# Optimization experiments

Measured on AMD Instinct MI355X. Metric: run time of the kernel, lower is better.

Reference implementation:

```python
import jax, jax.numpy as jnp
import numpy as np

LEAKY_SLOPE = 0.2

def leaky_relu(x):
    return jnp.where(x >= 0, x, LEAKY_SLOPE * x)

def setup_inputs() -> dict:
    key = jax.random.key(0)
    ks = jax.random.split(key, 11)
    B, F = 512, 1024
    H1, H2, OUT = 512, 256, 128  # hidden_dims = [512, 256, 128]
    KD = 5                        # minibatch kernel dims
    x = jax.random.normal(ks[0], (B, F), dtype=jnp.float32)
    # features: Linear(F,H1) -> LReLU -> Linear(H1,H2) -> LReLU
    W1 = jax.random.normal(ks[1], (F, H1), dtype=jnp.float32) / np.sqrt(F)
    b1 = jnp.zeros((H1,), dtype=jnp.float32)
    W2 = jax.random.normal(ks[2], (H1, H2), dtype=jnp.float32) / np.sqrt(H1)
    b2 = jnp.zeros((H2,), dtype=jnp.float32)
    # minibatch discrimination tensor T: (in=H2, out=OUT, kernel=KD), N(0,1) init
    T = jax.random.normal(ks[3], (H2, OUT, KD), dtype=jnp.float32)
    # final: Linear(H2+OUT, OUT) -> LReLU -> Linear(OUT, 1)
    W3 = jax.random.normal(ks[4], (H2 + OUT, OUT), dtype=jnp.float32) / np.sqrt(H2 + OUT)
    b3 = jnp.zeros((OUT,), dtype=jnp.float32)
    W4 = jax.random.normal(ks[5], (OUT, 1), dtype=jnp.float32) / np.sqrt(OUT)
    b4 = jnp.zeros((1,), dtype=jnp.float32)
    return {"x": x, "W1": W1, "b1": b1, "W2": W2, "b2": b2,
            "T": T, "W3": W3, "b3": b3, "W4": W4, "b4": b4}

def reference(x, W1, b1, W2, b2, T, W3, b3, W4, b4):
    # MLP feature stack (dropout = identity in eval mode)
    h = leaky_relu(x @ W1 + b1)          # (B, 512)
    h = leaky_relu(h @ W2 + b2)          # (B, 256)
    # Minibatch discrimination
    in_f, out_f, kd = T.shape
    M = (h @ T.reshape(in_f, out_f * kd)).reshape(-1, out_f, kd)  # (B, out, kd)
    # pairwise L1 over kernel dim: (B, B, out)
    norm = jnp.abs(M[:, None, :, :] - M[None, :, :, :]).sum(-1)
    o_b = jnp.exp(-norm).sum(0) - 1.0    # (B, out); -1 removes self term
    z = jnp.concatenate([h, o_b], axis=1)  # (B, 256+128)
    z = leaky_relu(z @ W3 + b3)
    return z @ W4 + b4                    # (B, 1)
```

## Files before the change

kernel.cpp:

```cpp
#include <hip/hip_runtime.h>
#include <math.h>

#define B_   512
#define F_   1024
#define H1_  512
#define H2_  256
#define OUT_ 128
#define KD_  5
#define NT_  640
#define ZK_  384

typedef short bf16x8 __attribute__((ext_vector_type(8)));
typedef float f32x16 __attribute__((ext_vector_type(16)));

__device__ __forceinline__ float lrelu(float v) { return v >= 0.f ? v : 0.2f * v; }

__device__ __forceinline__ unsigned f2bf(float f) {
    unsigned u = __float_as_uint(f);
    return (u + 0x7fffu + ((u >> 16) & 1u)) >> 16;
}
__device__ __forceinline__ unsigned pack2bf(float a, float b) {
    return f2bf(a) | (f2bf(b) << 16);
}

__device__ __forceinline__ bf16x8 frag_bf16row(const unsigned short* p, int idx, int ld, int k) {
    return *(const bf16x8*)(p + (size_t)idx * ld + k);
}
__device__ __forceinline__ bf16x8 frag_f32row(const float* p, int idx, int ld, int k) {
    const float4 a = *(const float4*)(p + (size_t)idx * ld + k);
    const float4 b = *(const float4*)(p + (size_t)idx * ld + k + 4);
    union { unsigned u[4]; bf16x8 v; } cv;
    cv.u[0] = pack2bf(a.x, a.y); cv.u[1] = pack2bf(a.z, a.w);
    cv.u[2] = pack2bf(b.x, b.y); cv.u[3] = pack2bf(b.z, b.w);
    return cv.v;
}
__device__ __forceinline__ bf16x8 frag_f32col(const float* p, int idx, int ld, int k) {
    union { unsigned u[4]; bf16x8 v; } cv;
    #pragma unroll
    for (int jj = 0; jj < 4; ++jj)
        cv.u[jj] = pack2bf(p[(size_t)(k + 2 * jj) * ld + idx],
                           p[(size_t)(k + 2 * jj + 1) * ld + idx]);
    return cv.v;
}
__device__ __forceinline__ bf16x8 frag_concat(const unsigned short* h2b,
                                              const float* obA, const float* obB,
                                              int idx, int k) {
    if (k < H2_) return frag_bf16row(h2b, idx, H2_, k);
    const float* pa = obA + (size_t)idx * OUT_ + (k - H2_);
    const float* pb = obB + (size_t)idx * OUT_ + (k - H2_);
    union { unsigned u[4]; bf16x8 v; } cv;
    #pragma unroll
    for (int jj = 0; jj < 4; ++jj)
        cv.u[jj] = pack2bf(pa[2 * jj] + pb[2 * jj], pa[2 * jj + 1] + pb[2 * jj + 1]);
    return cv.v;
}

#define M_BF16ROW 0
#define M_F32ROW  1
#define M_F32COL  2

template<int WAVES, int KSLICE, int AMODE, int BMODE,
         bool RELU, bool HAS_BIAS, bool BF16_OUT>
__global__ __launch_bounds__(WAVES * 64)
void gemm_k(const void* __restrict__ Ap, const void* __restrict__ Bp,
            const float* __restrict__ bias, void* __restrict__ Cout,
            int M, int N, int LDA, int LDB)
{
    __shared__ float Red[WAVES * 1024];
    const int tid  = threadIdx.x;
    const int wav  = tid >> 6;
    const int lane = tid & 63;
    const int half = lane >> 5;
    const int mn   = lane & 31;
    const int m0   = blockIdx.y * 32;
    const int n0   = blockIdx.x * 32;

    f32x16 acc;
    #pragma unroll
    for (int i = 0; i < 16; ++i) acc[i] = 0.f;

    #pragma unroll
    for (int s = 0; s < KSLICE / 16; ++s) {
        const int k = wav * KSLICE + 16 * s + 8 * half;
        bf16x8 af, bf;
        if (AMODE == M_BF16ROW)      af = frag_bf16row((const unsigned short*)Ap, m0 + mn, LDA, k);
        else if (AMODE == M_F32ROW)  af = frag_f32row((const float*)Ap, m0 + mn, LDA, k);
        else                         af = frag_f32col((const float*)Ap, m0 + mn, LDA, k);
        if (BMODE == M_BF16ROW)      bf = frag_bf16row((const unsigned short*)Bp, n0 + mn, LDB, k);
        else                         bf = frag_f32col((const float*)Bp, n0 + mn, LDB, k);
        acc = __builtin_amdgcn_mfma_f32_32x32x16_bf16(af, bf, acc, 0, 0, 0);
    }

    #pragma unroll
    for (int r = 0; r < 16; ++r) {
        const int row = (r & 3) + 8 * (r >> 2) + 4 * half;
        Red[wav * 1024 + row * 32 + mn] = acc[r];
    }
    __syncthreads();

    if (tid < 256) {
        const int e0 = tid * 4, row = e0 >> 5, col = e0 & 31;
        float v[4];
        #pragma unroll
        for (int q = 0; q < 4; ++q) {
            float u = 0.f;
            #pragma unroll
            for (int w = 0; w < WAVES; ++w) u += Red[w * 1024 + e0 + q];
            if (HAS_BIAS) u += bias[n0 + col + q];
            if (RELU) u = lrelu(u);
            v[q] = u;
        }
        if (BF16_OUT) {
            uint2 o;
            o.x = pack2bf(v[0], v[1]); o.y = pack2bf(v[2], v[3]);
            *(uint2*)((unsigned short*)Cout + (size_t)(m0 + row) * N + n0 + col) = o;
        } else {
            *(float4*)((float*)Cout + (size_t)(m0 + row) * N + n0 + col) =
                make_float4(v[0], v[1], v[2], v[3]);
        }
    }
}

__global__ __launch_bounds__(128)
void disc_kernel(const float* __restrict__ Mt, float* __restrict__ obH)
{
    const int o  = blockIdx.x >> 3;
    const int jq = (blockIdx.x >> 1) & 3;
    const int ih = blockIdx.x & 1;
    const int t  = threadIdx.x;
    const int j  = jq * 128 + t;
    const int i0 = ih * 256;
    __shared__ float L[256 * 8];
    const float* base = Mt + (size_t)o * 5 * 512;
    #pragma unroll
    for (int k = 0; k < KD_; ++k) {
        L[t * 8 + k]         = base[k * 512 + i0 + t];
        L[(t + 128) * 8 + k] = base[k * 512 + i0 + t + 128];
    }
    const float mj0 = base[0 * 512 + j], mj1 = base[1 * 512 + j],
                mj2 = base[2 * 512 + j], mj3 = base[3 * 512 + j],
                mj4 = base[4 * 512 + j];
    __syncthreads();

    float acc0 = 0.f, acc1 = 0.f;
    #pragma unroll 4
    for (int i = 0; i < 256; i += 2) {
        {
            const float4 a = *(const float4*)&L[i * 8];
            const float n = fabsf(a.x - mj0) + fabsf(a.y - mj1) + fabsf(a.z - mj2)
                          + fabsf(a.w - mj3) + fabsf(L[i * 8 + 4] - mj4);
            acc0 += __expf(-n);
        }
        {
            const float4 a = *(const float4*)&L[(i + 1) * 8];
            const float n = fabsf(a.x - mj0) + fabsf(a.y - mj1) + fabsf(a.z - mj2)
                          + fabsf(a.w - mj3) + fabsf(L[(i + 1) * 8 + 4] - mj4);
            acc1 += __expf(-n);
        }
    }
    const float self = ((j >> 8) == ih) ? 1.f : 0.f;
    obH[(size_t)ih * B_ * OUT_ + (size_t)j * OUT_ + o] = acc0 + acc1 - self;
}

__global__ __launch_bounds__(256)
void gemm3_dot(const unsigned short* __restrict__ h2b,
               const float* __restrict__ obA, const float* __restrict__ obB,
               const float* __restrict__ W3, const float* __restrict__ b3,
               const float* __restrict__ W4, const float* __restrict__ b4,
               float* __restrict__ out)
{
    __shared__ float Red[32 * 128];
    const int tid  = threadIdx.x;
    const int w    = tid >> 6;
    const int lane = tid & 63;
    const int half = lane >> 5;
    const int mn   = lane & 31;
    const int m0   = blockIdx.x * 32;
    const int n0   = w * 32;

    f32x16 acc;
    #pragma unroll
    for (int i = 0; i < 16; ++i) acc[i] = 0.f;

    #pragma unroll
    for (int s = 0; s < ZK_ / 16; ++s) {
        const int k = 16 * s + 8 * half;
        const bf16x8 af = frag_concat(h2b, obA, obB, m0 + mn, k);
        const bf16x8 bf = frag_f32col(W3, n0 + mn, OUT_, k);
        acc = __builtin_amdgcn_mfma_f32_32x32x16_bf16(af, bf, acc, 0, 0, 0);
    }

    #pragma unroll
    for (int r = 0; r < 16; ++r) {
        const int row = (r & 3) + 8 * (r >> 2) + 4 * half;
        const int col = n0 + mn;
        Red[row * 128 + col] = lrelu(acc[r] + b3[col]);
    }
    __syncthreads();

    if (tid < 128) {
        const int row = tid >> 2, q = tid & 3;
        float a = 0.f;
        #pragma unroll
        for (int cc0 = 0; cc0 < 32; ++cc0) {
            const int cc = (cc0 + tid) & 31;
            a += Red[row * 128 + q * 32 + cc] * W4[q * 32 + cc];
        }
        a += __shfl_down(a, 2, 4);
        a += __shfl_down(a, 1, 4);
        if (q == 0) out[m0 + row] = a + b4[0];
    }
}

extern "C" void kernel_launch(void* const* d_in, const int* in_sizes, int n_in,
                              void* d_out, int out_size, void* d_ws, size_t ws_size,
                              hipStream_t stream) {
    const float* x  = (const float*)d_in[0];
    const float* W1 = (const float*)d_in[1];
    const float* b1 = (const float*)d_in[2];
    const float* W2 = (const float*)d_in[3];
    const float* b2 = (const float*)d_in[4];
    const float* T  = (const float*)d_in[5];
    const float* W3 = (const float*)d_in[6];
    const float* b3 = (const float*)d_in[7];
    const float* W4 = (const float*)d_in[8];
    const float* b4 = (const float*)d_in[9];
    float* out = (float*)d_out;

    char* ws = (char*)d_ws;
    float*          Mt  = (float*)(ws + 0);
    float*          obH = (float*)(ws + 1310720);
    unsigned short* h1b = (unsigned short*)(ws + 1835008);
    unsigned short* h2b = (unsigned short*)(ws + 2359296);

    gemm_k<8, 128, M_F32ROW, M_F32COL, true, true, true>
        <<<dim3(H1_ / 32, B_ / 32), 512, 0, stream>>>(
        x, W1, b1, h1b, B_, H1_, F_, H1_);

    gemm_k<8, 64, M_BF16ROW, M_F32COL, true, true, true>
        <<<dim3(H2_ / 32, B_ / 32), 512, 0, stream>>>(
        h1b, W2, b2, h2b, B_, H2_, H1_, H2_);

    gemm_k<4, 64, M_F32COL, M_BF16ROW, false, false, false>
        <<<dim3(B_ / 32, NT_ / 32), 256, 0, stream>>>(
        T, h2b, nullptr, Mt, NT_, B_, NT_, H2_);

    disc_kernel<<<1024, 128, 0, stream>>>(Mt, obH);

    gemm3_dot<<<B_ / 32, 256, 0, stream>>>(
        h2b, obH, obH + B_ * OUT_, W3, b3, W4, b4, out);
}
```

Baseline: 109.3 us.

## Fuse all five stages into one cooperative persistent kernel with grid syncs

```diff
diff --git a/kernel.cpp b/kernel.cpp
--- a/kernel.cpp
+++ b/kernel.cpp
@@ -1,5 +1,8 @@
 #include <hip/hip_runtime.h>
+#include <hip/hip_cooperative_groups.h>
 #include <math.h>
+
+namespace cg = cooperative_groups;
 
 #define B_   512
 #define F_   1024
@@ -42,38 +45,22 @@
                            p[(size_t)(k + 2 * jj + 1) * ld + idx]);
     return cv.v;
 }
-__device__ __forceinline__ bf16x8 frag_concat(const unsigned short* h2b,
-                                              const float* obA, const float* obB,
-                                              int idx, int k) {
-    if (k < H2_) return frag_bf16row(h2b, idx, H2_, k);
-    const float* pa = obA + (size_t)idx * OUT_ + (k - H2_);
-    const float* pb = obB + (size_t)idx * OUT_ + (k - H2_);
-    union { unsigned u[4]; bf16x8 v; } cv;
-    #pragma unroll
-    for (int jj = 0; jj < 4; ++jj)
-        cv.u[jj] = pack2bf(pa[2 * jj] + pb[2 * jj], pa[2 * jj + 1] + pb[2 * jj + 1]);
-    return cv.v;
-}
 
 #define M_BF16ROW 0
 #define M_F32ROW  1
 #define M_F32COL  2
 
-template<int WAVES, int KSLICE, int AMODE, int BMODE,
-         bool RELU, bool HAS_BIAS, bool BF16_OUT>
-__global__ __launch_bounds__(WAVES * 64)
-void gemm_k(const void* __restrict__ Ap, const void* __restrict__ Bp,
-            const float* __restrict__ bias, void* __restrict__ Cout,
-            int M, int N, int LDA, int LDB)
-{
-    __shared__ float Red[WAVES * 1024];
-    const int tid  = threadIdx.x;
+template<int KSLICE, int AMODE, int BMODE, bool RELU, bool HAS_BIAS, bool BF16_OUT>
+__device__ __forceinline__
+void gemm_tile(float* Red,
+               const void* __restrict__ Ap, const void* __restrict__ Bp,
+               const float* __restrict__ bias, void* __restrict__ Cout,
+               int N, int LDA, int LDB, int m0, int n0, int tid)
+{
     const int wav  = tid >> 6;
     const int lane = tid & 63;
     const int half = lane >> 5;
     const int mn   = lane & 31;
-    const int m0   = blockIdx.y * 32;
-    const int n0   = blockIdx.x * 32;
 
     f32x16 acc;
     #pragma unroll
@@ -105,7 +92,7 @@
         for (int q = 0; q < 4; ++q) {
             float u = 0.f;
             #pragma unroll
-            for (int w = 0; w < WAVES; ++w) u += Red[w * 1024 + e0 + q];
+            for (int w = 0; w < 8; ++w) u += Red[w * 1024 + e0 + q];
             if (HAS_BIAS) u += bias[n0 + col + q];
             if (RELU) u = lrelu(u);
             v[q] = u;
@@ -119,73 +106,79 @@
                 make_float4(v[0], v[1], v[2], v[3]);
         }
     }
-}
-
-__global__ __launch_bounds__(128)
-void disc_kernel(const float* __restrict__ Mt, float* __restrict__ obH)
-{
-    const int o  = blockIdx.x >> 3;
-    const int jq = (blockIdx.x >> 1) & 3;
-    const int ih = blockIdx.x & 1;
-    const int t  = threadIdx.x;
-    const int j  = jq * 128 + t;
-    const int i0 = ih * 256;
-    __shared__ float L[256 * 8];
-    const float* base = Mt + (size_t)o * 5 * 512;
-    #pragma unroll
-    for (int k = 0; k < KD_; ++k) {
-        L[t * 8 + k]         = base[k * 512 + i0 + t];
-        L[(t + 128) * 8 + k] = base[k * 512 + i0 + t + 128];
-    }
+    __syncthreads();
+}
+
+__device__ __forceinline__
+void disc_phase(float* S, const float* __restrict__ Mt, float* __restrict__ obF,
+                int b, int tid)
+{
+    float* L = S;
+    float* P = S + 4096;
+    const int o  = b >> 1;
+    const int jh = b & 1;
+    const int t  = tid & 255;
+    const int ih = tid >> 8;
+    const float* base = Mt + (size_t)o * (KD_ * 512);
+
+    #pragma unroll
+    for (int k = 0; k < KD_; ++k)
+        L[tid * 8 + k] = base[k * 512 + tid];
+
+    const int j = jh * 256 + t;
     const float mj0 = base[0 * 512 + j], mj1 = base[1 * 512 + j],
                 mj2 = base[2 * 512 + j], mj3 = base[3 * 512 + j],
                 mj4 = base[4 * 512 + j];
     __syncthreads();
 
+    const int i0 = ih * 256;
     float acc0 = 0.f, acc1 = 0.f;
     #pragma unroll 4
     for (int i = 0; i < 256; i += 2) {
         {
-            const float4 a = *(const float4*)&L[i * 8];
+            const float4 a = *(const float4*)&L[(i0 + i) * 8];
             const float n = fabsf(a.x - mj0) + fabsf(a.y - mj1) + fabsf(a.z - mj2)
-                          + fabsf(a.w - mj3) + fabsf(L[i * 8 + 4] - mj4);
+                          + fabsf(a.w - mj3) + fabsf(L[(i0 + i) * 8 + 4] - mj4);
             acc0 += __expf(-n);
         }
         {
-            const float4 a = *(const float4*)&L[(i + 1) * 8];
+            const float4 a = *(const float4*)&L[(i0 + i + 1) * 8];
             const float n = fabsf(a.x - mj0) + fabsf(a.y - mj1) + fabsf(a.z - mj2)
-                          + fabsf(a.w - mj3) + fabsf(L[(i + 1) * 8 + 4] - mj4);
+                          + fabsf(a.w - mj3) + fabsf(L[(i0 + i + 1) * 8 + 4] - mj4);
             acc1 += __expf(-n);
         }
     }
-    const float self = ((j >> 8) == ih) ? 1.f : 0.f;
-    obH[(size_t)ih * B_ * OUT_ + (size_t)j * OUT_ + o] = acc0 + acc1 - self;
-}
-
-__global__ __launch_bounds__(256)
-void gemm3_dot(const unsigned short* __restrict__ h2b,
-               const float* __restrict__ obA, const float* __restrict__ obB,
-               const float* __restrict__ W3, const float* __restrict__ b3,
-               const float* __restrict__ W4, const float* __restrict__ b4,
-               float* __restrict__ out)
-{
-    __shared__ float Red[32 * 128];
-    const int tid  = threadIdx.x;
+    if (ih == 0) P[t] = acc0 + acc1;
+    __syncthreads();
+    if (ih == 1) obF[(size_t)o * B_ + j] = P[t] + acc0 + acc1 - 1.0f;
+    __syncthreads();
+}
+
+__device__ __forceinline__
+void final_phase(float* Red, const unsigned short* __restrict__ h2b,
+                 const float* __restrict__ obF,
+                 const float* __restrict__ W3, const float* __restrict__ b3,
+                 const float* __restrict__ W4, const float* __restrict__ b4,
+                 float* __restrict__ out, int m0, int tid)
+{
     const int w    = tid >> 6;
     const int lane = tid & 63;
     const int half = lane >> 5;
     const int mn   = lane & 31;
-    const int m0   = blockIdx.x * 32;
-    const int n0   = w * 32;
+    const int n0   = (w & 3) * 32;
+    const int kh   = w >> 2;
 
     f32x16 acc;
     #pragma unroll
     for (int i = 0; i < 16; ++i) acc[i] = 0.f;
 
     #pragma unroll
-    for (int s = 0; s < ZK_ / 16; ++s) {
-        const int k = 16 * s + 8 * half;
-        const bf16x8 af = frag_concat(h2b, obA, obB, m0 + mn, k);
+    for (int s = 0; s < 12; ++s) {
+        const int k = kh * 192 + 16 * s + 8 * half;
+        const int idx = m0 + mn;
+        bf16x8 af;
+        if (k < H2_) af = frag_bf16row(h2b, idx, H2_, k);
+        else         af = frag_f32col(obF, idx, B_, k - H2_);
         const bf16x8 bf = frag_f32col(W3, n0 + mn, OUT_, k);
         acc = __builtin_amdgcn_mfma_f32_32x32x16_bf16(af, bf, acc, 0, 0, 0);
     }
@@ -193,8 +186,7 @@
     #pragma unroll
     for (int r = 0; r < 16; ++r) {
         const int row = (r & 3) + 8 * (r >> 2) + 4 * half;
-        const int col = n0 + mn;
-        Red[row * 128 + col] = lrelu(acc[r] + b3[col]);
+        Red[kh * 4096 + row * 128 + n0 + mn] = acc[r];
     }
     __syncthreads();
 
@@ -204,12 +196,50 @@
         #pragma unroll
         for (int cc0 = 0; cc0 < 32; ++cc0) {
             const int cc = (cc0 + tid) & 31;
-            a += Red[row * 128 + q * 32 + cc] * W4[q * 32 + cc];
+            const int c = q * 32 + cc;
+            const float u = lrelu(Red[row * 128 + c] + Red[4096 + row * 128 + c] + b3[c]);
+            a += u * W4[c];
         }
         a += __shfl_down(a, 2, 4);
         a += __shfl_down(a, 1, 4);
         if (q == 0) out[m0 + row] = a + b4[0];
     }
+}
+
+__global__ __launch_bounds__(512)
+void mega(const float* __restrict__ x,  const float* __restrict__ W1, const float* __restrict__ b1,
+          const float* __restrict__ W2, const float* __restrict__ b2,
+          const float* __restrict__ T,
+          const float* __restrict__ W3, const float* __restrict__ b3,
+          const float* __restrict__ W4, const float* __restrict__ b4,
+          float* __restrict__ Mt, float* __restrict__ obF,
+          unsigned short* __restrict__ h1b, unsigned short* __restrict__ h2b,
+          float* __restrict__ out)
+{
+    __shared__ float S[8192];
+    cg::grid_group grid = cg::this_grid();
+    const int b   = blockIdx.x;
+    const int tid = threadIdx.x;
+
+    gemm_tile<128, M_F32ROW, M_F32COL, true, true, true>(
+        S, x, W1, b1, h1b, H1_, F_, H1_, (b >> 4) * 32, (b & 15) * 32, tid);
+    __threadfence(); grid.sync();
+
+    if (b < 128)
+        gemm_tile<64, M_BF16ROW, M_F32COL, true, true, true>(
+            S, h1b, W2, b2, h2b, H2_, H1_, H2_, (b >> 3) * 32, (b & 7) * 32, tid);
+    __threadfence(); grid.sync();
+
+    for (int t = b; t < 320; t += 256)
+        gemm_tile<32, M_F32COL, M_BF16ROW, false, false, false>(
+            S, T, h2b, nullptr, Mt, B_, NT_, H2_, (t / 16) * 32, (t % 16) * 32, tid);
+    __threadfence(); grid.sync();
+
+    disc_phase(S, Mt, obF, b, tid);
+    __threadfence(); grid.sync();
+
+    if (b < 16)
+        final_phase(S, h2b, obF, W3, b3, W4, b4, out, b * 32, tid);
 }
 
 extern "C" void kernel_launch(void* const* d_in, const int* in_sizes, int n_in,
@@ -229,24 +259,12 @@
 
     char* ws = (char*)d_ws;
     float*          Mt  = (float*)(ws + 0);
-    float*          obH = (float*)(ws + 1310720);
-    unsigned short* h1b = (unsigned short*)(ws + 1835008);
-    unsigned short* h2b = (unsigned short*)(ws + 2359296);
-
-    gemm_k<8, 128, M_F32ROW, M_F32COL, true, true, true>
-        <<<dim3(H1_ / 32, B_ / 32), 512, 0, stream>>>(
-        x, W1, b1, h1b, B_, H1_, F_, H1_);
-
-    gemm_k<8, 64, M_BF16ROW, M_F32COL, true, true, true>
-        <<<dim3(H2_ / 32, B_ / 32), 512, 0, stream>>>(
-        h1b, W2, b2, h2b, B_, H2_, H1_, H2_);
-
-    gemm_k<4, 64, M_F32COL, M_BF16ROW, false, false, false>
-        <<<dim3(B_ / 32, NT_ / 32), 256, 0, stream>>>(
-        T, h2b, nullptr, Mt, NT_, B_, NT_, H2_);
-
-    disc_kernel<<<1024, 128, 0, stream>>>(Mt, obH);
-
-    gemm3_dot<<<B_ / 32, 256, 0, stream>>>(
-        h2b, obH, obH + B_ * OUT_, W3, b3, W4, b4, out);
-}
+    float*          obF = (float*)(ws + 1310720);
+    unsigned short* h1b = (unsigned short*)(ws + 1572864);
+    unsigned short* h2b = (unsigned short*)(ws + 2097152);
+
+    void* args[] = { (void*)&x,  (void*)&W1, (void*)&b1, (void*)&W2, (void*)&b2,
+                     (void*)&T,  (void*)&W3, (void*)&b3, (void*)&W4, (void*)&b4,
+                     (void*)&Mt, (void*)&obF, (void*)&h1b, (void*)&h2b, (void*)&out };
+    hipLaunchCooperativeKernel((const void*)mega, dim3(256), dim3(512), args, 0, stream);
+}
```

Measured after the change: 388.9 us. 3.56x slower.

## Fuse minibatch projection GEMM into discrimination kernel, dropping Mt buffer

Applied to the files above, without the earlier changes.

```diff
diff --git a/kernel.cpp b/kernel.cpp
--- a/kernel.cpp
+++ b/kernel.cpp
@@ -121,45 +121,79 @@
     }
 }
 
-__global__ __launch_bounds__(128)
-void disc_kernel(const float* __restrict__ Mt, float* __restrict__ obH)
+__global__ __launch_bounds__(512)
+void discM2_kernel(const unsigned short* __restrict__ h2b,
+                   const float* __restrict__ T,
+                   float* __restrict__ obH)
 {
-    const int o  = blockIdx.x >> 3;
-    const int jq = (blockIdx.x >> 1) & 3;
-    const int ih = blockIdx.x & 1;
-    const int t  = threadIdx.x;
-    const int j  = jq * 128 + t;
+    __shared__ float Msl[512 * 8];
+    const int b    = blockIdx.x;
+    const int o    = b >> 1;
+    const int ih   = b & 1;
+    const int tid  = threadIdx.x;
+    const int w    = tid >> 6;
+    const int lane = tid & 63;
+    const int half = lane >> 5;
+    const int mn   = lane & 31;
+
+    const float* Tc = T + (size_t)o * KD_ + mn;
+    const bool   tc_ok = (mn < KD_);
+
+    const int m0 = w * 64;
+    f32x16 acc0, acc1;
+    #pragma unroll
+    for (int i = 0; i < 16; ++i) { acc0[i] = 0.f; acc1[i] = 0.f; }
+
+    #pragma unroll 4
+    for (int s = 0; s < 16; ++s) {
+        const int k = 16 * s + 8 * half;
+        union { unsigned u[4]; bf16x8 v; } cv;
+        cv.u[0] = 0u; cv.u[1] = 0u; cv.u[2] = 0u; cv.u[3] = 0u;
+        if (tc_ok) {
+            #pragma unroll
+            for (int jj = 0; jj < 4; ++jj)
+                cv.u[jj] = pack2bf(Tc[(size_t)(k + 2 * jj) * NT_],
+                                   Tc[(size_t)(k + 2 * jj + 1) * NT_]);
+        }
+        const bf16x8 bfr = cv.v;
+        const bf16x8 a0 = frag_bf16row(h2b, m0 + mn, H2_, k);
+        const bf16x8 a1 = frag_bf16row(h2b, m0 + 32 + mn, H2_, k);
+        acc0 = __builtin_amdgcn_mfma_f32_32x32x16_bf16(a0, bfr, acc0, 0, 0, 0);
+        acc1 = __builtin_amdgcn_mfma_f32_32x32x16_bf16(a1, bfr, acc1, 0, 0, 0);
+    }
+    #pragma unroll
+    for (int r = 0; r < 16; ++r) {
+        const int row = (r & 3) + 8 * (r >> 2) + 4 * half;
+        if (tc_ok) {
+            Msl[(m0 + row) * 8 + mn]      = acc0[r];
+            Msl[(m0 + 32 + row) * 8 + mn] = acc1[r];
+        }
+    }
+    __syncthreads();
+
+    const int j = tid;
+    const float mj0 = Msl[j * 8 + 0], mj1 = Msl[j * 8 + 1], mj2 = Msl[j * 8 + 2],
+                mj3 = Msl[j * 8 + 3], mj4 = Msl[j * 8 + 4];
     const int i0 = ih * 256;
-    __shared__ float L[256 * 8];
-    const float* base = Mt + (size_t)o * 5 * 512;
-    #pragma unroll
-    for (int k = 0; k < KD_; ++k) {
-        L[t * 8 + k]         = base[k * 512 + i0 + t];
-        L[(t + 128) * 8 + k] = base[k * 512 + i0 + t + 128];
-    }
-    const float mj0 = base[0 * 512 + j], mj1 = base[1 * 512 + j],
-                mj2 = base[2 * 512 + j], mj3 = base[3 * 512 + j],
-                mj4 = base[4 * 512 + j];
-    __syncthreads();
-
-    float acc0 = 0.f, acc1 = 0.f;
+
+    float acca = 0.f, accb = 0.f;
     #pragma unroll 4
     for (int i = 0; i < 256; i += 2) {
         {
-            const float4 a = *(const float4*)&L[i * 8];
+            const float4 a = *(const float4*)&Msl[(i0 + i) * 8];
             const float n = fabsf(a.x - mj0) + fabsf(a.y - mj1) + fabsf(a.z - mj2)
-                          + fabsf(a.w - mj3) + fabsf(L[i * 8 + 4] - mj4);
-            acc0 += __expf(-n);
+                          + fabsf(a.w - mj3) + fabsf(Msl[(i0 + i) * 8 + 4] - mj4);
+            acca += __expf(-n);
         }
         {
-            const float4 a = *(const float4*)&L[(i + 1) * 8];
+            const float4 a = *(const float4*)&Msl[(i0 + i + 1) * 8];
             const float n = fabsf(a.x - mj0) + fabsf(a.y - mj1) + fabsf(a.z - mj2)
-                          + fabsf(a.w - mj3) + fabsf(L[(i + 1) * 8 + 4] - mj4);
-            acc1 += __expf(-n);
+                          + fabsf(a.w - mj3) + fabsf(Msl[(i0 + i + 1) * 8 + 4] - mj4);
+            accb += __expf(-n);
         }
     }
     const float self = ((j >> 8) == ih) ? 1.f : 0.f;
-    obH[(size_t)ih * B_ * OUT_ + (size_t)j * OUT_ + o] = acc0 + acc1 - self;
+    obH[(size_t)ih * B_ * OUT_ + (size_t)j * OUT_ + o] = acca + accb - self;
 }
 
 __global__ __launch_bounds__(256)
@@ -186,8 +220,8 @@
     for (int s = 0; s < ZK_ / 16; ++s) {
         const int k = 16 * s + 8 * half;
         const bf16x8 af = frag_concat(h2b, obA, obB, m0 + mn, k);
-        const bf16x8 bf = frag_f32col(W3, n0 + mn, OUT_, k);
-        acc = __builtin_amdgcn_mfma_f32_32x32x16_bf16(af, bf, acc, 0, 0, 0);
+        const bf16x8 bfr = frag_f32col(W3, n0 + mn, OUT_, k);
+        acc = __builtin_amdgcn_mfma_f32_32x32x16_bf16(af, bfr, acc, 0, 0, 0);
     }
 
     #pragma unroll
@@ -228,10 +262,9 @@
     float* out = (float*)d_out;
 
     char* ws = (char*)d_ws;
-    float*          Mt  = (float*)(ws + 0);
-    float*          obH = (float*)(ws + 1310720);
-    unsigned short* h1b = (unsigned short*)(ws + 1835008);
-    unsigned short* h2b = (unsigned short*)(ws + 2359296);
+    float*          obH = (float*)(ws + 0);
+    unsigned short* h1b = (unsigned short*)(ws + 524288);
+    unsigned short* h2b = (unsigned short*)(ws + 1048576);
 
     gemm_k<8, 128, M_F32ROW, M_F32COL, true, true, true>
         <<<dim3(H1_ / 32, B_ / 32), 512, 0, stream>>>(
@@ -241,11 +274,7 @@
         <<<dim3(H2_ / 32, B_ / 32), 512, 0, stream>>>(
         h1b, W2, b2, h2b, B_, H2_, H1_, H2_);
 
-    gemm_k<4, 64, M_F32COL, M_BF16ROW, false, false, false>
-        <<<dim3(B_ / 32, NT_ / 32), 256, 0, stream>>>(
-        T, h2b, nullptr, Mt, NT_, B_, NT_, H2_);
-
-    disc_kernel<<<1024, 128, 0, stream>>>(Mt, obH);
+    discM2_kernel<<<256, 512, 0, stream>>>(h2b, T, obH);
 
     gemm3_dot<<<B_ / 32, 256, 0, stream>>>(
         h2b, obH, obH + B_ * OUT_, W3, b3, W4, b4, out);
```

After: 117.5 us. 1.08x slower.

## Pre-transpose and convert weights and input to bf16 in a prep kernel

Applied to the files above, without the earlier changes.

```diff
diff --git a/kernel.cpp b/kernel.cpp
--- a/kernel.cpp
+++ b/kernel.cpp
@@ -26,22 +26,6 @@
 __device__ __forceinline__ bf16x8 frag_bf16row(const unsigned short* p, int idx, int ld, int k) {
     return *(const bf16x8*)(p + (size_t)idx * ld + k);
 }
-__device__ __forceinline__ bf16x8 frag_f32row(const float* p, int idx, int ld, int k) {
-    const float4 a = *(const float4*)(p + (size_t)idx * ld + k);
-    const float4 b = *(const float4*)(p + (size_t)idx * ld + k + 4);
-    union { unsigned u[4]; bf16x8 v; } cv;
-    cv.u[0] = pack2bf(a.x, a.y); cv.u[1] = pack2bf(a.z, a.w);
-    cv.u[2] = pack2bf(b.x, b.y); cv.u[3] = pack2bf(b.z, b.w);
-    return cv.v;
-}
-__device__ __forceinline__ bf16x8 frag_f32col(const float* p, int idx, int ld, int k) {
-    union { unsigned u[4]; bf16x8 v; } cv;
-    #pragma unroll
-    for (int jj = 0; jj < 4; ++jj)
-        cv.u[jj] = pack2bf(p[(size_t)(k + 2 * jj) * ld + idx],
-                           p[(size_t)(k + 2 * jj + 1) * ld + idx]);
-    return cv.v;
-}
 __device__ __forceinline__ bf16x8 frag_concat(const unsigned short* h2b,
                                               const float* obA, const float* obB,
                                               int idx, int k) {
@@ -55,16 +39,50 @@
     return cv.v;
 }
 
-#define M_BF16ROW 0
-#define M_F32ROW  1
-#define M_F32COL  2
-
-template<int WAVES, int KSLICE, int AMODE, int BMODE,
-         bool RELU, bool HAS_BIAS, bool BF16_OUT>
+__global__ __launch_bounds__(256)
+void prep_kernel(const float* __restrict__ x,  const float* __restrict__ W1,
+                 const float* __restrict__ W2, const float* __restrict__ T,
+                 const float* __restrict__ W3,
+                 unsigned short* __restrict__ xb,  unsigned short* __restrict__ W1t,
+                 unsigned short* __restrict__ W2t, unsigned short* __restrict__ Tt,
+                 unsigned short* __restrict__ W3t)
+{
+    __shared__ float L[32][33];
+    const int b = blockIdx.x, tid = threadIdx.x;
+    if (b < 848) {
+        const float* in; unsigned short* outp; int R, C, tile;
+        if (b < 512)      { in = W1; outp = W1t; R = 1024; C = 512; tile = b; }
+        else if (b < 640) { in = W2; outp = W2t; R = 512;  C = 256; tile = b - 512; }
+        else if (b < 800) { in = T;  outp = Tt;  R = 256;  C = 640; tile = b - 640; }
+        else              { in = W3; outp = W3t; R = 384;  C = 128; tile = b - 800; }
+        const int nc = C >> 5;
+        const int r0 = (tile / nc) * 32, c0 = (tile % nc) * 32;
+        const int lr = tid >> 3, lc = (tid & 7) * 4;
+        const float4 v = *(const float4*)(in + (size_t)(r0 + lr) * C + c0 + lc);
+        L[lr][lc + 0] = v.x; L[lr][lc + 1] = v.y;
+        L[lr][lc + 2] = v.z; L[lr][lc + 3] = v.w;
+        __syncthreads();
+        const int orow = tid >> 3, ocol = (tid & 7) * 4;
+        uint2 o;
+        o.x = pack2bf(L[ocol + 0][orow], L[ocol + 1][orow]);
+        o.y = pack2bf(L[ocol + 2][orow], L[ocol + 3][orow]);
+        *(uint2*)(outp + (size_t)(c0 + orow) * R + r0 + ocol) = o;
+    } else {
+        const int e = (b - 848) * 2048 + tid * 8;
+        const float4 a = *(const float4*)(x + e);
+        const float4 c = *(const float4*)(x + e + 4);
+        uint4 o;
+        o.x = pack2bf(a.x, a.y); o.y = pack2bf(a.z, a.w);
+        o.z = pack2bf(c.x, c.y); o.w = pack2bf(c.z, c.w);
+        *(uint4*)(xb + e) = o;
+    }
+}
+
+template<int WAVES, int KSLICE, bool RELU, bool HAS_BIAS, bool BF16_OUT>
 __global__ __launch_bounds__(WAVES * 64)
-void gemm_k(const void* __restrict__ Ap, const void* __restrict__ Bp,
+void gemm_k(const unsigned short* __restrict__ Ap, const unsigned short* __restrict__ Bp,
             const float* __restrict__ bias, void* __restrict__ Cout,
-            int M, int N, int LDA, int LDB)
+            int N, int LDA, int LDB)
 {
     __shared__ float Red[WAVES * 1024];
     const int tid  = threadIdx.x;
@@ -82,12 +100,8 @@
     #pragma unroll
     for (int s = 0; s < KSLICE / 16; ++s) {
         const int k = wav * KSLICE + 16 * s + 8 * half;
-        bf16x8 af, bf;
-        if (AMODE == M_BF16ROW)      af = frag_bf16row((const unsigned short*)Ap, m0 + mn, LDA, k);
-        else if (AMODE == M_F32ROW)  af = frag_f32row((const float*)Ap, m0 + mn, LDA, k);
-        else                         af = frag_f32col((const float*)Ap, m0 + mn, LDA, k);
-        if (BMODE == M_BF16ROW)      bf = frag_bf16row((const unsigned short*)Bp, n0 + mn, LDB, k);
-        else                         bf = frag_f32col((const float*)Bp, n0 + mn, LDB, k);
+        const bf16x8 af = frag_bf16row(Ap, m0 + mn, LDA, k);
+        const bf16x8 bf = frag_bf16row(Bp, n0 + mn, LDB, k);
         acc = __builtin_amdgcn_mfma_f32_32x32x16_bf16(af, bf, acc, 0, 0, 0);
     }
 
@@ -165,7 +179,7 @@
 __global__ __launch_bounds__(256)
 void gemm3_dot(const unsigned short* __restrict__ h2b,
                const float* __restrict__ obA, const float* __restrict__ obB,
-               const float* __restrict__ W3, const float* __restrict__ b3,
+               const unsigned short* __restrict__ W3t, const float* __restrict__ b3,
                const float* __restrict__ W4, const float* __restrict__ b4,
                float* __restrict__ out)
 {
@@ -185,9 +199,9 @@
     #pragma unroll
     for (int s = 0; s < ZK_ / 16; ++s) {
         const int k = 16 * s + 8 * half;
-        const bf16x8 af = frag_concat(h2b, obA, obB, m0 + mn, k);
-        const bf16x8 bf = frag_f32col(W3, n0 + mn, OUT_, k);
-        acc = __builtin_amdgcn_mfma_f32_32x32x16_bf16(af, bf, acc, 0, 0, 0);
+        const bf16x8 af  = frag_concat(h2b, obA, obB, m0 + mn, k);
+        const bf16x8 bfr = frag_bf16row(W3t, n0 + mn, ZK_, k);
+        acc = __builtin_amdgcn_mfma_f32_32x32x16_bf16(af, bfr, acc, 0, 0, 0);
     }
 
     #pragma unroll
@@ -232,21 +246,28 @@
     float*          obH = (float*)(ws + 1310720);
     unsigned short* h1b = (unsigned short*)(ws + 1835008);
     unsigned short* h2b = (unsigned short*)(ws + 2359296);
-
-    gemm_k<8, 128, M_F32ROW, M_F32COL, true, true, true>
+    unsigned short* xb  = (unsigned short*)(ws + 2621440);
+    unsigned short* W1t = (unsigned short*)(ws + 3670016);
+    unsigned short* W2t = (unsigned short*)(ws + 4718592);
+    unsigned short* Tt  = (unsigned short*)(ws + 4980736);
+    unsigned short* W3t = (unsigned short*)(ws + 5308416);
+
+    prep_kernel<<<1104, 256, 0, stream>>>(x, W1, W2, T, W3, xb, W1t, W2t, Tt, W3t);
+
+    gemm_k<8, 128, true, true, true>
         <<<dim3(H1_ / 32, B_ / 32), 512, 0, stream>>>(
-        x, W1, b1, h1b, B_, H1_, F_, H1_);
-
-    gemm_k<8, 64, M_BF16ROW, M_F32COL, true, true, true>
+        xb, W1t, b1, h1b, H1_, F_, F_);
+
+    gemm_k<8, 64, true, true, true>
         <<<dim3(H2_ / 32, B_ / 32), 512, 0, stream>>>(
-        h1b, W2, b2, h2b, B_, H2_, H1_, H2_);
-
-    gemm_k<4, 64, M_F32COL, M_BF16ROW, false, false, false>
+        h1b, W2t, b2, h2b, H2_, H1_, H1_);
+
+    gemm_k<4, 64, false, false, false>
         <<<dim3(B_ / 32, NT_ / 32), 256, 0, stream>>>(
-        T, h2b, nullptr, Mt, NT_, B_, NT_, H2_);
+        Tt, h2b, nullptr, Mt, B_, H2_, H2_);
 
     disc_kernel<<<1024, 128, 0, stream>>>(Mt, obH);
 
     gemm3_dot<<<B_ / 32, 256, 0, stream>>>(
-        h2b, obH, obH + B_ * OUT_, W3, b3, W4, b4, out);
-}
+        h2b, obH, obH + B_ * OUT_, W3t, b3, W4, b4, out);
+}
```

After: 115.2 us. +5.4%, slower.
